# Performance work log

Measured on AMD Instinct MI355X. Metric: run time of the kernel, lower is better.

## Reference

```python
import jax, jax.numpy as jnp
import numpy as np

L = 2000          # per-modality dialogue length (all_dia_len)
M = 3             # num_modal
F = 512           # feature_size
E = 400000        # number of edges (<= 500000 edge_weight params)
N = M * L         # total nodes
NUM_LAYERS = 2
EW_SIZE = 500000
W_SCALE = 0.044   # ~1/sqrt(F) to keep activations sane


def setup_inputs() -> dict:
    key = jax.random.key(0)
    ks = jax.random.split(key, 9)
    x_a = jax.random.normal(ks[0], (L, F), jnp.float32)
    x_v = jax.random.normal(ks[1], (L, F), jnp.float32)
    x_t = jax.random.normal(ks[2], (L, F), jnp.float32)
    edge_index = jax.random.randint(ks[3], (2, E), 0, N, dtype=jnp.int32)
    edge_weight_param = jnp.ones((EW_SIZE,), jnp.float32)
    gcn_W = jax.random.normal(ks[4], (NUM_LAYERS, F, F), jnp.float32) * W_SCALE
    gcn_b = jnp.zeros((NUM_LAYERS, F), jnp.float32)
    fc_W = jax.random.normal(ks[5], (NUM_LAYERS, F, F), jnp.float32) * W_SCALE
    fc_b = jnp.zeros((NUM_LAYERS, F), jnp.float32)
    return {
        "x_a": x_a, "x_v": x_v, "x_t": x_t,
        "edge_weight_param": edge_weight_param,
        "gcn_W": gcn_W, "gcn_b": gcn_b,
        "fc_W": fc_W, "fc_b": fc_b,
        "edge_index": edge_index,
    }


def _gcn_fact(edge_index, edge_weight, num_nodes):
    # sparse edge list -> dense adjacency (scatter-add, duplicate edges coalesce)
    adj = jnp.zeros((num_nodes, num_nodes), edge_weight.dtype)
    adj = adj.at[edge_index[0], edge_index[1]].add(edge_weight)
    row_sum = adj.sum(axis=1)
    # torch: pow(row_sum, -0.5), inf -> 0  (safe form for zero-degree nodes)
    pos = row_sum > 0
    d_inv_sqrt = jnp.where(pos, jax.lax.rsqrt(jnp.where(pos, row_sum, 1.0)), 0.0)
    # D^{-1/2} A D^{-1/2} via row/col broadcast (same math as diag matmuls)
    return d_inv_sqrt[:, None] * adj * d_inv_sqrt[None, :]


def reference(x_a, x_v, x_t, edge_weight_param, gcn_W, gcn_b, fc_W, fc_b, edge_index):
    feature = jnp.concatenate([x_a, x_v, x_t], axis=0)      # [N, F]
    edge_weight = edge_weight_param[: edge_index.shape[1]]   # [E]
    gcn = _gcn_fact(edge_index, edge_weight, feature.shape[0])
    feature_sum = feature
    for i in range(NUM_LAYERS):
        # encoder layer: one dense GCN propagation + projection
        feature = jax.nn.relu(gcn @ feature @ gcn_W[i] + gcn_b[i])
        # fc layer: Linear + LeakyReLU (dropout = identity at eval)
        feature_sum = feature_sum + jax.nn.leaky_relu(feature @ fc_W[i] + fc_b[i], 0.01)
    # chunk back into per-modality features
    return tuple(jnp.split(feature_sum, M, axis=0))
```

## Files before the change

### kernel.cpp

```cpp
#include <hip/hip_runtime.h>
#include <hip/hip_bf16.h>

#define LL 2000
#define MM 3
#define FF 512
#define NN (MM * LL)
#define NUM_LAYERS 2

typedef __attribute__((ext_vector_type(8))) short bf16x8;
typedef __attribute__((ext_vector_type(4))) float f32x4;

__device__ __forceinline__ unsigned short f2bf(float x) {
    __hip_bfloat16 b = __float2bfloat16(x);
    return *(unsigned short*)&b;
}

__device__ __forceinline__ void gload16(const void* gsrc, void* ldst) {
    __builtin_amdgcn_global_load_lds((const __attribute__((address_space(1))) unsigned int*)gsrc,
                                     (__attribute__((address_space(3))) unsigned int*)ldst,
                                     16, 0, 0);
}

__global__ void concat_init(const float* __restrict__ xa,
                            const float* __restrict__ xv,
                            const float* __restrict__ xt,
                            unsigned short* __restrict__ feat,
                            float* __restrict__ out_sum) {
    int idx4 = blockIdx.x * blockDim.x + threadIdx.x;
    const int per4 = (LL * FF) / 4;
    if (idx4 >= 3 * per4) return;
    const float4* src;
    int off;
    if (idx4 < per4)            { src = (const float4*)xa; off = idx4; }
    else if (idx4 < 2 * per4)   { src = (const float4*)xv; off = idx4 - per4; }
    else                        { src = (const float4*)xt; off = idx4 - 2 * per4; }
    float4 v = src[off];
    ((float4*)out_sum)[idx4] = v;
    ushort4 pk;
    pk.x = f2bf(v.x); pk.y = f2bf(v.y); pk.z = f2bf(v.z); pk.w = f2bf(v.w);
    ((ushort4*)feat)[idx4] = pk;
}

__global__ __launch_bounds__(256) void wtrans(const float* __restrict__ gcnW,
                                              const float* __restrict__ fcW,
                                              unsigned short* __restrict__ Wt) {
    int mz = blockIdx.z;
    int layer = (mz < 2) ? mz : mz - 2;
    const float* src = (mz < 2) ? (gcnW + (size_t)layer * FF * FF)
                                : (fcW + (size_t)layer * FF * FF);
    int slot = (mz < 2) ? (mz * 2) : ((mz - 2) * 2 + 1);
    unsigned short* dst = Wt + (size_t)slot * FF * FF;
    __shared__ unsigned short tile[64][65];
    int k0 = blockIdx.x * 64;
    int n0 = blockIdx.y * 64;
    int tid = threadIdx.x;
    for (int i = tid; i < 64 * 64; i += 256) {
        int r = i >> 6, c = i & 63;
        tile[r][c] = f2bf(src[(size_t)(k0 + r) * FF + n0 + c]);
    }
    __syncthreads();
    for (int i = tid; i < 64 * 64; i += 256) {
        int r = i >> 6, c = i & 63;
        dst[(size_t)(n0 + r) * FF + k0 + c] = tile[c][r];
    }
}

__global__ void edge_count(const int* __restrict__ src,
                           int* __restrict__ counts,
                           int* __restrict__ pir, int E) {
    int e = blockIdx.x * blockDim.x + threadIdx.x;
    if (e >= E) return;
    pir[e] = atomicAdd(&counts[src[e]], 1);
}

__global__ __launch_bounds__(1024) void scan_kernel(const int* __restrict__ counts,
                                                    int* __restrict__ row_start, int n) {
    __shared__ int partial[1024];
    int t = threadIdx.x;
    const int chunk = (n + 1023) / 1024;
    int base = t * chunk;
    int s = 0;
    for (int i = 0; i < chunk; i++)
        if (base + i < n) s += counts[base + i];
    partial[t] = s;
    __syncthreads();
    for (int off = 1; off < 1024; off <<= 1) {
        int add = (t >= off) ? partial[t - off] : 0;
        __syncthreads();
        partial[t] += add;
        __syncthreads();
    }
    int excl = (t == 0) ? 0 : partial[t - 1];
    for (int i = 0; i < chunk; i++) {
        if (base + i < n) { row_start[base + i] = excl; excl += counts[base + i]; }
    }
    if (t == 1023) row_start[n] = partial[1023];
}

__global__ void scatter_kernel(const int* __restrict__ src,
                               const int* __restrict__ dst,
                               const float* __restrict__ wparam,
                               const int* __restrict__ row_start,
                               const int* __restrict__ pir,
                               int2* __restrict__ csr, int E) {
    int e = blockIdx.x * blockDim.x + threadIdx.x;
    if (e >= E) return;
    int r = src[e];
    int2 p;
    p.x = dst[e];
    p.y = __float_as_int(wparam[e]);
    csr[row_start[r] + pir[e]] = p;
}

__global__ __launch_bounds__(256) void rowsum_dinv(const int2* __restrict__ csr,
                                                   const int* __restrict__ row_start,
                                                   float* __restrict__ dinv) {
    int wave = threadIdx.x >> 6, lane = threadIdx.x & 63;
    int r = blockIdx.x * 4 + wave;
    int s = row_start[r], e = row_start[r + 1];
    float sum = 0.0f;
    for (int i = s + lane; i < e; i += 64) sum += __int_as_float(csr[i].y);
#pragma unroll
    for (int off = 32; off > 0; off >>= 1) sum += __shfl_xor(sum, off);
    if (lane == 0) dinv[r] = (sum > 0.0f) ? rsqrtf(sum) : 0.0f;
}

__global__ void fixup_kernel(int2* __restrict__ csr,
                             const float* __restrict__ dinv, int nnz) {
    int i = blockIdx.x * blockDim.x + threadIdx.x;
    if (i >= nnz) return;
    int2 p = csr[i];
    p.y = __float_as_int(__int_as_float(p.y) * dinv[p.x]);
    csr[i] = p;
}

__device__ __forceinline__ void accum8(float* acc, uint4 h, float v) {
    unsigned int d[4] = {h.x, h.y, h.z, h.w};
#pragma unroll
    for (int k = 0; k < 4; k++) {
        float lo = __uint_as_float(d[k] << 16);
        float hi = __uint_as_float(d[k] & 0xFFFF0000u);
        acc[2 * k]     = fmaf(v, lo, acc[2 * k]);
        acc[2 * k + 1] = fmaf(v, hi, acc[2 * k + 1]);
    }
}

__global__ __launch_bounds__(256) void spmm_bias_relu(const unsigned short* __restrict__ H,
                                                      const int* __restrict__ row_start,
                                                      const int2* __restrict__ csr,
                                                      const float* __restrict__ dinv,
                                                      const float* __restrict__ bias,
                                                      unsigned short* __restrict__ featOut) {
    int wave = threadIdx.x >> 6, lane = threadIdx.x & 63;
    int r = blockIdx.x * 4 + wave;
    int s = row_start[r], e = row_start[r + 1];
    int f0 = lane * 8;
    const unsigned short* Hf = H + f0;
    float acc[8] = {0, 0, 0, 0, 0, 0, 0, 0};

    int i = s;
    int2 p0, p1, p2, p3;
    bool have = (i + 4 <= e);
    if (have) { p0 = csr[i]; p1 = csr[i + 1]; p2 = csr[i + 2]; p3 = csr[i + 3]; }
    while (have) {
        uint4 a0 = *(const uint4*)(Hf + (size_t)p0.x * FF);
        uint4 a1 = *(const uint4*)(Hf + (size_t)p1.x * FF);
        uint4 a2 = *(const uint4*)(Hf + (size_t)p2.x * FF);
        uint4 a3 = *(const uint4*)(Hf + (size_t)p3.x * FF);
        float v0 = __int_as_float(p0.y), v1 = __int_as_float(p1.y);
        float v2 = __int_as_float(p2.y), v3 = __int_as_float(p3.y);
        i += 4;
        have = (i + 4 <= e);
        if (have) { p0 = csr[i]; p1 = csr[i + 1]; p2 = csr[i + 2]; p3 = csr[i + 3]; }
        accum8(acc, a0, v0);
        accum8(acc, a1, v1);
        accum8(acc, a2, v2);
        accum8(acc, a3, v3);
    }
    for (; i < e; i++) {
        int2 p = csr[i];
        uint4 a = *(const uint4*)(Hf + (size_t)p.x * FF);
        accum8(acc, a, __int_as_float(p.y));
    }

    float dr = dinv[r];
    float4 b0 = *(const float4*)(bias + f0);
    float4 b1 = *(const float4*)(bias + f0 + 4);
    float bb[8] = {b0.x, b0.y, b0.z, b0.w, b1.x, b1.y, b1.z, b1.w};
    unsigned int o[4];
#pragma unroll
    for (int k = 0; k < 4; k++) {
        float v0 = fmaxf(fmaf(acc[2 * k], dr, bb[2 * k]), 0.0f);
        float v1 = fmaxf(fmaf(acc[2 * k + 1], dr, bb[2 * k + 1]), 0.0f);
        o[k] = (unsigned int)f2bf(v0) | ((unsigned int)f2bf(v1) << 16);
    }
    uint4 ov; ov.x = o[0]; ov.y = o[1]; ov.z = o[2]; ov.w = o[3];
    *(uint4*)(featOut + (size_t)r * FF + f0) = ov;
}

template <int MODE>
__global__ __launch_bounds__(256) void gemm_bf16(const unsigned short* __restrict__ A,
                                                 const unsigned short* __restrict__ Bt,
                                                 const float* __restrict__ fbias,
                                                 unsigned short* __restrict__ Hout,
                                                 float* __restrict__ out,
                                                 int M) {
    __shared__ short As[64 * 64];
    __shared__ short Bs[64 * 64];
    int tid = threadIdx.x;
    int wave = tid >> 6;
    int lane = tid & 63;
    int lane16 = lane & 15;
    int quad = lane >> 4;
    int m0 = blockIdx.x * 64;
    int n0 = blockIdx.y * 64;
    int wm = (wave >> 1) * 32;
    int wn = (wave & 1) * 32;

    f32x4 acc[2][2] = {};

    for (int k0 = 0; k0 < FF; k0 += 64) {
#pragma unroll
        for (int s = 0; s < 2; s++) {
            int c = wave * 128 + s * 64 + lane;
            int row = c >> 3;
            int kcs = c & 7;
            int kc = kcs ^ (row & 7);
            int ar = m0 + row; if (ar >= M) ar = 0;
            const short* ga = (const short*)A + (size_t)ar * FF + k0 + kc * 8;
            gload16(ga, &As[(wave * 128 + s * 64) * 8]);
            const short* gb = (const short*)Bt + (size_t)(n0 + row) * FF + k0 + kc * 8;
            gload16(gb, &Bs[(wave * 128 + s * 64) * 8]);
        }
        __syncthreads();
#pragma unroll
        for (int kk = 0; kk < 2; kk++) {
            bf16x8 a[2], b[2];
#pragma unroll
            for (int mt = 0; mt < 2; mt++) {
                int row = wm + mt * 16 + lane16;
                int kc = kk * 4 + quad;
                int kcs = kc ^ (row & 7);
                a[mt] = *(const bf16x8*)&As[row * 64 + kcs * 8];
            }
#pragma unroll
            for (int nt = 0; nt < 2; nt++) {
                int row = wn + nt * 16 + lane16;
                int kc = kk * 4 + quad;
                int kcs = kc ^ (row & 7);
                b[nt] = *(const bf16x8*)&Bs[row * 64 + kcs * 8];
            }
#pragma unroll
            for (int mt = 0; mt < 2; mt++)
#pragma unroll
                for (int nt = 0; nt < 2; nt++)
                    acc[mt][nt] = __builtin_amdgcn_mfma_f32_16x16x32_bf16(a[mt], b[nt], acc[mt][nt], 0, 0, 0);
        }
        __syncthreads();
    }

    bool isFc = (MODE == 1) || (MODE == 2 && n0 < FF);
#pragma unroll
    for (int mt = 0; mt < 2; mt++) {
#pragma unroll
        for (int nt = 0; nt < 2; nt++) {
            int n = n0 + wn + nt * 16 + lane16;
            float bv = isFc ? fbias[(MODE == 2) ? n : n] : 0.0f;
#pragma unroll
            for (int rr = 0; rr < 4; rr++) {
                int m = m0 + wm + mt * 16 + quad * 4 + rr;
                if (m < M) {
                    float v = acc[mt][nt][rr];
                    if (isFc) {
                        v += bv;
                        v = (v > 0.0f) ? v : 0.01f * v;
                        out[(size_t)m * FF + n] += v;
                    } else {
                        int nc = (MODE == 2) ? (n - FF) : n;
                        Hout[(size_t)m * FF + nc] = f2bf(v);
                    }
                }
            }
        }
    }
}

extern "C" void kernel_launch(void* const* d_in, const int* in_sizes, int n_in,
                              void* d_out, int out_size, void* d_ws, size_t ws_size,
                              hipStream_t stream) {
    const float* xa      = (const float*)d_in[0];
    const float* xv      = (const float*)d_in[1];
    const float* xt      = (const float*)d_in[2];
    const float* ew      = (const float*)d_in[3];
    const float* gcn_W   = (const float*)d_in[4];
    const float* gcn_b   = (const float*)d_in[5];
    const float* fc_W    = (const float*)d_in[6];
    const float* fc_b    = (const float*)d_in[7];
    const int*   eidx    = (const int*)d_in[8];
    const int E = in_sizes[8] / 2;
    const int* esrc = eidx;
    const int* edst = eidx + E;

    float* out = (float*)d_out;

    char* w = (char*)d_ws;
    int*   counts    = (int*)  (w + 0);
    int*   row_start = (int*)  (w + 24064);
    float* dinv      = (float*)(w + 48128);
    int2*  csr       = (int2*) (w + 72192);
    unsigned short* feat = (unsigned short*)(w + 3272192);
    unsigned short* H    = (unsigned short*)(w + 9416192);
    unsigned short* Wt   = (unsigned short*)(w + 15560192);
    int*   pir       = (int*)H;

    hipMemsetAsync(counts, 0, 24000, stream);

    {
        int tot4 = (NN * FF) / 4;
        concat_init<<<(tot4 + 255) / 256, 256, 0, stream>>>(xa, xv, xt, feat, out);
    }
    wtrans<<<dim3(FF / 64, FF / 64, 4), 256, 0, stream>>>(gcn_W, fc_W, Wt);

    edge_count<<<(E + 255) / 256, 256, 0, stream>>>(esrc, counts, pir, E);
    scan_kernel<<<1, 1024, 0, stream>>>(counts, row_start, NN);
    scatter_kernel<<<(E + 255) / 256, 256, 0, stream>>>(esrc, edst, ew, row_start, pir, csr, E);
    rowsum_dinv<<<NN / 4, 256, 0, stream>>>(csr, row_start, dinv);
    fixup_kernel<<<(E + 255) / 256, 256, 0, stream>>>(csr, dinv, E);

    const int gx = (NN + 63) / 64;
    gemm_bf16<0><<<dim3(gx, 8), 256, 0, stream>>>(feat, Wt, nullptr, H, nullptr, NN);
    spmm_bias_relu<<<NN / 4, 256, 0, stream>>>(H, row_start, csr, dinv, gcn_b, feat);
    gemm_bf16<2><<<dim3(gx, 16), 256, 0, stream>>>(feat, Wt + (size_t)FF * FF, fc_b, H, out, NN);
    spmm_bias_relu<<<NN / 4, 256, 0, stream>>>(H, row_start, csr, dinv, gcn_b + FF, feat);
    gemm_bf16<1><<<dim3(gx, 8), 256, 0, stream>>>(feat, Wt + (size_t)3 * FF * FF, fc_b + FF, nullptr, out, NN);
}
```

Measured before the change: 229.4 us.

## Fuse prep kernels, enlarge GEMM M-tile, split SpMM rows across feature halves

Merges concat/bf16 conversion, weight transpose and edge counting into one prep kernel, removing two launches. The GEMM block tile grows from 64 to 128 rows, so each wave computes 4x2 MFMA tiles and B-tile loads are reused across more rows. The SpMM now assigns half a wave to each row and splits the features into two 256-wide halves across blocks, meant to improve load balance and parallelism on short rows. The cost is more registers and shared memory per GEMM block and fewer GEMM blocks, which can lower occupancy on a grid of only about 47 M-tiles.

Measured after the change: 234.4 us. 1.02x slower.

```diff
diff --git a/kernel.cpp b/kernel.cpp
--- a/kernel.cpp
+++ b/kernel.cpp
@@ -21,56 +21,57 @@
                                      16, 0, 0);
 }
 
-__global__ void concat_init(const float* __restrict__ xa,
-                            const float* __restrict__ xv,
-                            const float* __restrict__ xt,
-                            unsigned short* __restrict__ feat,
-                            float* __restrict__ out_sum) {
-    int idx4 = blockIdx.x * blockDim.x + threadIdx.x;
-    const int per4 = (LL * FF) / 4;
-    if (idx4 >= 3 * per4) return;
-    const float4* src;
-    int off;
-    if (idx4 < per4)            { src = (const float4*)xa; off = idx4; }
-    else if (idx4 < 2 * per4)   { src = (const float4*)xv; off = idx4 - per4; }
-    else                        { src = (const float4*)xt; off = idx4 - 2 * per4; }
-    float4 v = src[off];
-    ((float4*)out_sum)[idx4] = v;
-    ushort4 pk;
-    pk.x = f2bf(v.x); pk.y = f2bf(v.y); pk.z = f2bf(v.z); pk.w = f2bf(v.w);
-    ((ushort4*)feat)[idx4] = pk;
-}
-
-__global__ __launch_bounds__(256) void wtrans(const float* __restrict__ gcnW,
-                                              const float* __restrict__ fcW,
-                                              unsigned short* __restrict__ Wt) {
-    int mz = blockIdx.z;
-    int layer = (mz < 2) ? mz : mz - 2;
-    const float* src = (mz < 2) ? (gcnW + (size_t)layer * FF * FF)
-                                : (fcW + (size_t)layer * FF * FF);
-    int slot = (mz < 2) ? (mz * 2) : ((mz - 2) * 2 + 1);
-    unsigned short* dst = Wt + (size_t)slot * FF * FF;
+__global__ __launch_bounds__(256) void prep(const float* __restrict__ xa,
+                                            const float* __restrict__ xv,
+                                            const float* __restrict__ xt,
+                                            unsigned short* __restrict__ feat,
+                                            float* __restrict__ out_sum,
+                                            const float* __restrict__ gcnW,
+                                            const float* __restrict__ fcW,
+                                            unsigned short* __restrict__ Wt,
+                                            const int* __restrict__ esrc,
+                                            int* __restrict__ counts,
+                                            int* __restrict__ pir, int E) {
     __shared__ unsigned short tile[64][65];
-    int k0 = blockIdx.x * 64;
-    int n0 = blockIdx.y * 64;
+    int b = blockIdx.x;
     int tid = threadIdx.x;
-    for (int i = tid; i < 64 * 64; i += 256) {
-        int r = i >> 6, c = i & 63;
-        tile[r][c] = f2bf(src[(size_t)(k0 + r) * FF + n0 + c]);
-    }
-    __syncthreads();
-    for (int i = tid; i < 64 * 64; i += 256) {
-        int r = i >> 6, c = i & 63;
-        dst[(size_t)(n0 + r) * FF + k0 + c] = tile[c][r];
-    }
-}
-
-__global__ void edge_count(const int* __restrict__ src,
-                           int* __restrict__ counts,
-                           int* __restrict__ pir, int E) {
-    int e = blockIdx.x * blockDim.x + threadIdx.x;
-    if (e >= E) return;
-    pir[e] = atomicAdd(&counts[src[e]], 1);
+    if (b < 3000) {
+        int idx4 = b * 256 + tid;
+        const int per4 = (LL * FF) / 4;
+        const float4* src;
+        int off;
+        if (idx4 < per4)            { src = (const float4*)xa; off = idx4; }
+        else if (idx4 < 2 * per4)   { src = (const float4*)xv; off = idx4 - per4; }
+        else                        { src = (const float4*)xt; off = idx4 - 2 * per4; }
+        float4 v = src[off];
+        ((float4*)out_sum)[idx4] = v;
+        ushort4 pk;
+        pk.x = f2bf(v.x); pk.y = f2bf(v.y); pk.z = f2bf(v.z); pk.w = f2bf(v.w);
+        ((ushort4*)feat)[idx4] = pk;
+    } else if (b < 3256) {
+        int idx = b - 3000;
+        int mz = idx >> 6;
+        int rem = idx & 63;
+        int k0 = (rem >> 3) * 64;
+        int n0 = (rem & 7) * 64;
+        int layer = (mz < 2) ? mz : mz - 2;
+        const float* src = (mz < 2) ? (gcnW + (size_t)layer * FF * FF)
+                                    : (fcW + (size_t)layer * FF * FF);
+        int slot = (mz < 2) ? (mz * 2) : ((mz - 2) * 2 + 1);
+        unsigned short* dst = Wt + (size_t)slot * FF * FF;
+        for (int i = tid; i < 64 * 64; i += 256) {
+            int r = i >> 6, c = i & 63;
+            tile[r][c] = f2bf(src[(size_t)(k0 + r) * FF + n0 + c]);
+        }
+        __syncthreads();
+        for (int i = tid; i < 64 * 64; i += 256) {
+            int r = i >> 6, c = i & 63;
+            dst[(size_t)(n0 + r) * FF + k0 + c] = tile[c][r];
+        }
+    } else {
+        int e = (b - 3256) * 256 + tid;
+        if (e < E) pir[e] = atomicAdd(&counts[esrc[e]], 1);
+    }
 }
 
 __global__ __launch_bounds__(1024) void scan_kernel(const int* __restrict__ counts,
@@ -152,10 +153,14 @@
                                                       const float* __restrict__ bias,
                                                       unsigned short* __restrict__ featOut) {
     int wave = threadIdx.x >> 6, lane = threadIdx.x & 63;
-    int r = blockIdx.x * 4 + wave;
+    int half = blockIdx.x & 1;
+    int rowbase = (blockIdx.x >> 1) * 8;
+    int sub = lane >> 5;
+    int l = lane & 31;
+    int r = rowbase + wave * 2 + sub;
+    int f0 = half * 256 + l * 8;
+    const unsigned short* Hf = H + f0;
     int s = row_start[r], e = row_start[r + 1];
-    int f0 = lane * 8;
-    const unsigned short* Hf = H + f0;
     float acc[8] = {0, 0, 0, 0, 0, 0, 0, 0};
 
     int i = s;
@@ -205,53 +210,56 @@
                                                  unsigned short* __restrict__ Hout,
                                                  float* __restrict__ out,
                                                  int M) {
-    __shared__ short As[64 * 64];
+    __shared__ short As[128 * 64];
     __shared__ short Bs[64 * 64];
     int tid = threadIdx.x;
     int wave = tid >> 6;
     int lane = tid & 63;
     int lane16 = lane & 15;
     int quad = lane >> 4;
-    int m0 = blockIdx.x * 64;
+    int m0 = blockIdx.x * 128;
     int n0 = blockIdx.y * 64;
-    int wm = (wave >> 1) * 32;
+    int wm = (wave >> 1) * 64;
     int wn = (wave & 1) * 32;
 
-    f32x4 acc[2][2] = {};
+    f32x4 acc[4][2] = {};
 
     for (int k0 = 0; k0 < FF; k0 += 64) {
 #pragma unroll
-        for (int s = 0; s < 2; s++) {
-            int c = wave * 128 + s * 64 + lane;
+        for (int it = 0; it < 4; it++) {
+            int c = it * 256 + tid;
             int row = c >> 3;
-            int kcs = c & 7;
-            int kc = kcs ^ (row & 7);
-            int ar = m0 + row; if (ar >= M) ar = 0;
-            const short* ga = (const short*)A + (size_t)ar * FF + k0 + kc * 8;
-            gload16(ga, &As[(wave * 128 + s * 64) * 8]);
-            const short* gb = (const short*)Bt + (size_t)(n0 + row) * FF + k0 + kc * 8;
-            gload16(gb, &Bs[(wave * 128 + s * 64) * 8]);
+            int kc = (c & 7) ^ (row & 7);
+            int ar = m0 + row; if (ar >= M) ar = M - 1;
+            gload16((const short*)A + (size_t)ar * FF + k0 + kc * 8,
+                    &As[(it * 256 + wave * 64) * 8]);
+        }
+#pragma unroll
+        for (int it = 0; it < 2; it++) {
+            int c = it * 256 + tid;
+            int row = c >> 3;
+            int kc = (c & 7) ^ (row & 7);
+            gload16((const short*)Bt + (size_t)(n0 + row) * FF + k0 + kc * 8,
+                    &Bs[(it * 256 + wave * 64) * 8]);
         }
         __syncthreads();
 #pragma unroll
         for (int kk = 0; kk < 2; kk++) {
-            bf16x8 a[2], b[2];
-#pragma unroll
-            for (int mt = 0; mt < 2; mt++) {
+            bf16x8 a[4], b[2];
+#pragma unroll
+            for (int mt = 0; mt < 4; mt++) {
                 int row = wm + mt * 16 + lane16;
-                int kc = kk * 4 + quad;
-                int kcs = kc ^ (row & 7);
-                a[mt] = *(const bf16x8*)&As[row * 64 + kcs * 8];
+                int kc = (kk * 4 + quad) ^ (row & 7);
+                a[mt] = *(const bf16x8*)&As[row * 64 + kc * 8];
             }
 #pragma unroll
             for (int nt = 0; nt < 2; nt++) {
                 int row = wn + nt * 16 + lane16;
-                int kc = kk * 4 + quad;
-                int kcs = kc ^ (row & 7);
-                b[nt] = *(const bf16x8*)&Bs[row * 64 + kcs * 8];
+                int kc = (kk * 4 + quad) ^ (row & 7);
+                b[nt] = *(const bf16x8*)&Bs[row * 64 + kc * 8];
             }
 #pragma unroll
-            for (int mt = 0; mt < 2; mt++)
+            for (int mt = 0; mt < 4; mt++)
 #pragma unroll
                 for (int nt = 0; nt < 2; nt++)
                     acc[mt][nt] = __builtin_amdgcn_mfma_f32_16x16x32_bf16(a[mt], b[nt], acc[mt][nt], 0, 0, 0);
@@ -261,11 +269,11 @@
 
     bool isFc = (MODE == 1) || (MODE == 2 && n0 < FF);
 #pragma unroll
-    for (int mt = 0; mt < 2; mt++) {
+    for (int mt = 0; mt < 4; mt++) {
 #pragma unroll
         for (int nt = 0; nt < 2; nt++) {
             int n = n0 + wn + nt * 16 + lane16;
-            float bv = isFc ? fbias[(MODE == 2) ? n : n] : 0.0f;
+            float bv = isFc ? fbias[n] : 0.0f;
 #pragma unroll
             for (int rr = 0; rr < 4; rr++) {
                 int m = m0 + wm + mt * 16 + quad * 4 + rr;
@@ -315,22 +323,18 @@
 
     hipMemsetAsync(counts, 0, 24000, stream);
 
-    {
-        int tot4 = (NN * FF) / 4;
-        concat_init<<<(tot4 + 255) / 256, 256, 0, stream>>>(xa, xv, xt, feat, out);
-    }
-    wtrans<<<dim3(FF / 64, FF / 64, 4), 256, 0, stream>>>(gcn_W, fc_W, Wt);
-
-    edge_count<<<(E + 255) / 256, 256, 0, stream>>>(esrc, counts, pir, E);
+    const int eblocks = (E + 255) / 256;
+    prep<<<3256 + eblocks, 256, 0, stream>>>(xa, xv, xt, feat, out,
+                                             gcn_W, fc_W, Wt, esrc, counts, pir, E);
     scan_kernel<<<1, 1024, 0, stream>>>(counts, row_start, NN);
-    scatter_kernel<<<(E + 255) / 256, 256, 0, stream>>>(esrc, edst, ew, row_start, pir, csr, E);
+    scatter_kernel<<<eblocks, 256, 0, stream>>>(esrc, edst, ew, row_start, pir, csr, E);
     rowsum_dinv<<<NN / 4, 256, 0, stream>>>(csr, row_start, dinv);
-    fixup_kernel<<<(E + 255) / 256, 256, 0, stream>>>(csr, dinv, E);
-
-    const int gx = (NN + 63) / 64;
+    fixup_kernel<<<eblocks, 256, 0, stream>>>(csr, dinv, E);
+
+    const int gx = (NN + 127) / 128;
     gemm_bf16<0><<<dim3(gx, 8), 256, 0, stream>>>(feat, Wt, nullptr, H, nullptr, NN);
-    spmm_bias_relu<<<NN / 4, 256, 0, stream>>>(H, row_start, csr, dinv, gcn_b, feat);
+    spmm_bias_relu<<<(NN / 8) * 2, 256, 0, stream>>>(H, row_start, csr, dinv, gcn_b, feat);
     gemm_bf16<2><<<dim3(gx, 16), 256, 0, stream>>>(feat, Wt + (size_t)FF * FF, fc_b, H, out, NN);
-    spmm_bias_relu<<<NN / 4, 256, 0, stream>>>(H, row_start, csr, dinv, gcn_b + FF, feat);
+    spmm_bias_relu<<<(NN / 8) * 2, 256, 0, stream>>>(H, row_start, csr, dinv, gcn_b + FF, feat);
     gemm_bf16<1><<<dim3(gx, 8), 256, 0, stream>>>(feat, Wt + (size_t)3 * FF * FF, fc_b + FF, nullptr, out, NN);
 }
```
